# Kernel optimization log

Measured on AMD Instinct MI355X. Metric: run time of the kernel, lower is better.

## Reference

```python
import jax, jax.numpy as jnp
import numpy as np

B, N = 1, 512
CS, CZ = 384, 128
H, DQK, DV, PQK, PV = 12, 16, 16, 4, 8
EPS = 1e-8
SW = float(np.sqrt(1.0 / (3 * DQK)))            # scalar_weights
PW = float(np.sqrt(1.0 / (3 * PQK * 9.0 / 2)))  # point_weights
ZW = float(np.sqrt(1.0 / 3))                    # attention_2d_weights


def _lin(key, din, dout):
    return 0.02 * jax.random.normal(key, (din, dout), dtype=jnp.float32), jnp.zeros((dout,), dtype=jnp.float32)


def setup_inputs():
    key = jax.random.key(0)
    ks = jax.random.split(key, 16)
    Wsq, bsq = _lin(ks[0], CS, H * DQK)
    Wsk, bsk = _lin(ks[1], CS, H * DQK)
    Wsv, bsv = _lin(ks[2], CS, H * DV)
    Wsb, bsb = _lin(ks[3], CZ, H)
    Wpq, bpq = _lin(ks[4], CS, H * PQK * 3)
    Wpk, bpk = _lin(ks[5], CS, H * PQK * 3)
    Wpv, bpv = _lin(ks[6], CS, H * PV * 3)
    Wout, bout = _lin(ks[7], H * (DV + PV * 4 + CZ), CS)
    w_attn = 0.5 * jax.random.normal(ks[8], (3,), dtype=jnp.float32)  # attn_linear weight (1,3)
    b_attn = jnp.zeros((), dtype=jnp.float32)
    tpw = jnp.full((H,), float(np.log(np.e - 1.0)), dtype=jnp.float32)  # trainable_point_weight
    s = jax.random.normal(ks[9], (B, N, CS), dtype=jnp.float32)
    z = jax.random.normal(ks[10], (B, N, N, CZ), dtype=jnp.float32)
    rot = jax.random.normal(ks[11], (B, N, 3, 3), dtype=jnp.float32)
    tran = jax.random.normal(ks[12], (B, N, 3), dtype=jnp.float32)
    res_mask = jnp.ones((B, N), dtype=jnp.float32)
    return dict(s=s, z=z, rot=rot, tran=tran, res_mask=res_mask,
                Wsq=Wsq, bsq=bsq, Wsk=Wsk, bsk=bsk, Wsv=Wsv, bsv=bsv,
                Wsb=Wsb, bsb=bsb, Wpq=Wpq, bpq=bpq, Wpk=Wpk, bpk=bpk,
                Wpv=Wpv, bpv=bpv, w_attn=w_attn, b_attn=b_attn, tpw=tpw,
                Wout=Wout, bout=bout)


def _ipa(s, z, rot, tran, res_mask, Wsq, bsq, Wsk, bsk, Wsv, bsv, Wsb, bsb,
         Wpq, bpq, Wpk, bpk, Wpv, bpv, w_attn, b_attn, tpw, Wout, bout):
    b, n, _ = s.shape
    sq = (s @ Wsq + bsq).reshape(b, n, H, DQK)
    sk = (s @ Wsk + bsk).reshape(b, n, H, DQK)
    sv = (s @ Wsv + bsv).reshape(b, n, H, DV)
    sb = z @ Wsb + bsb  # [b, i, j, h] pair bias

    def to_global(W, bias, p):
        t = (s @ W + bias).reshape(b, n, H, p, 3)
        return jnp.einsum('bnxy,bnhpy->bnhpx', rot, t) + tran[:, :, None, None, :]

    pqg = to_global(Wpq, bpq, PQK)
    pkg = to_global(Wpk, bpk, PQK)
    pvg = to_global(Wpv, bpv, PV)

    diff = pqg[:, :, None] - pkg[:, None, :]          # [b, i, j, h, p, 3]
    sdist = jnp.sum(diff * diff, axis=(-1, -2))       # [b, i, j, h]

    attn_point = -0.5 * jax.nn.softplus(tpw) * sdist * PW
    attn_scalar = jnp.einsum('bihd,bjhd->bijh', sq * SW, sk)
    attn_pair = sb * ZW
    # attn_linear(stack([scalar, point, pair], -1)).squeeze(-1)
    logits = attn_scalar * w_attn[0] + attn_point * w_attn[1] + attn_pair * w_attn[2] + b_attn

    mask2d = res_mask[:, :, None] * res_mask[:, None, :]
    logits = jnp.where(mask2d[..., None] == 0, jnp.finfo(logits.dtype).min, logits)
    attn = jax.nn.softmax(logits, axis=2)             # softmax over j

    r_scalar = jnp.einsum('bijh,bjhd->bihd', attn, sv)
    r_pt_g = jnp.einsum('bijh,bjhpc->bihpc', attn, pvg)
    # rotate back to local frame: R^T (x - t)
    r_pt = jnp.einsum('biyx,bihpy->bihpx', rot, r_pt_g - tran[:, :, None, None, :])
    r_norm = jnp.sqrt(jnp.sum(r_pt * r_pt, axis=-1) + EPS)  # [b, i, h, p]
    r_pair = jnp.einsum('bijh,bijc->bihc', attn, z)

    cat = jnp.concatenate([r_scalar, r_pt.reshape(b, n, H, PV * 3), r_norm, r_pair], axis=-1)
    return cat.reshape(b, n, -1) @ Wout + bout


def reference(s, z, rot, tran, res_mask, Wsq, bsq, Wsk, bsk, Wsv, bsv, Wsb, bsb,
              Wpq, bpq, Wpk, bpk, Wpv, bpv, w_attn, b_attn, tpw, Wout, bout):
    return _ipa(s, z, rot, tran, res_mask, Wsq, bsq, Wsk, bsk, Wsv, bsv, Wsb, bsb,
                Wpq, bpq, Wpk, bpk, Wpv, bpv, w_attn, b_attn, tpw, Wout, bout)
```

## Files before the change

kernel.cpp:

```cpp
#include <hip/hip_runtime.h>
#include <hip/hip_bf16.h>
#include <math.h>

#define NN 512
#define CSD 384
#define CZ 128
#define HH 12
#define TMPW 1152
#define CATH 176
#define CATDIM 2112
#define NSPLIT 6
#define KSPL 352

#define SW 0.14433756729740643f
#define PW 0.13608276348795434f
#define ZW 0.57735026918962576f
#define NEG_INF -3.4028234663852886e38f

typedef float f32x4_t __attribute__((ext_vector_type(4)));
typedef short bf16x8_t __attribute__((ext_vector_type(8)));

union BFU { uint4 q; bf16x8_t v; ushort u[8]; };

static __device__ __forceinline__ ushort f2bf(float f) {
    __hip_bfloat16 h = __float2bfloat16(f);
    return *reinterpret_cast<ushort*>(&h);
}
static __device__ __forceinline__ float bf2f(ushort u) {
    unsigned int v = ((unsigned int)u) << 16;
    return __uint_as_float(v);
}

__global__ void proj_gemm_kernel(const float* __restrict__ s, const float* __restrict__ rot,
                                 const float* __restrict__ tran,
                                 const float* __restrict__ Wsq, const float* __restrict__ bsq,
                                 const float* __restrict__ Wsk, const float* __restrict__ bsk,
                                 const float* __restrict__ Wsv, const float* __restrict__ bsv,
                                 const float* __restrict__ Wpq, const float* __restrict__ bpq,
                                 const float* __restrict__ Wpk, const float* __restrict__ bpk,
                                 const float* __restrict__ Wpv, const float* __restrict__ bpv,
                                 float* __restrict__ tmp)
{
    int bx = blockIdx.x;
    int n0 = blockIdx.y * 32;
    int f0 = bx * 48;
    const float* W; const float* bb; int dout; int segstart;
    if (bx < 4)       { W = Wsq; bb = bsq; dout = 192; segstart = 0; }
    else if (bx < 8)  { W = Wsk; bb = bsk; dout = 192; segstart = 192; }
    else if (bx < 12) { W = Wsv; bb = bsv; dout = 192; segstart = 384; }
    else if (bx < 15) { W = Wpq; bb = bpq; dout = 144; segstart = 576; }
    else if (bx < 18) { W = Wpk; bb = bpk; dout = 144; segstart = 720; }
    else              { W = Wpv; bb = bpv; dout = 288; segstart = 864; }
    int colbase = f0 - segstart;

    __shared__ float St[32][34];
    __shared__ float Ws[32][49];
    int tid = threadIdx.x;
    int ty = tid >> 4, tx = tid & 15;
    float acc[2][3] = {{0,0,0},{0,0,0}};

    for (int k0 = 0; k0 < CSD; k0 += 32) {
        {
            int r = tid >> 3, c4 = (tid & 7) * 4;
            float4 v = *(const float4*)&s[(size_t)(n0 + r) * CSD + k0 + c4];
            St[c4 + 0][r] = v.x; St[c4 + 1][r] = v.y; St[c4 + 2][r] = v.z; St[c4 + 3][r] = v.w;
        }
        for (int e = tid; e < 1536; e += 256) {
            int r = e / 48, c = e % 48;
            Ws[r][c] = W[(size_t)(k0 + r) * dout + colbase + c];
        }
        __syncthreads();
        #pragma unroll
        for (int k = 0; k < 32; k++) {
            float2 a = *(const float2*)&St[k][ty * 2];
            float b0 = Ws[k][tx * 3], b1 = Ws[k][tx * 3 + 1], b2 = Ws[k][tx * 3 + 2];
            acc[0][0] += a.x * b0; acc[0][1] += a.x * b1; acc[0][2] += a.x * b2;
            acc[1][0] += a.y * b0; acc[1][1] += a.y * b1; acc[1][2] += a.y * b2;
        }
        __syncthreads();
    }
    float bv0 = bb[colbase + tx * 3], bv1 = bb[colbase + tx * 3 + 1], bv2 = bb[colbase + tx * 3 + 2];
    #pragma unroll
    for (int r = 0; r < 2; r++) {
        int n = n0 + ty * 2 + r;
        float v0 = acc[r][0] + bv0, v1 = acc[r][1] + bv1, v2 = acc[r][2] + bv2;
        float* o = tmp + (size_t)n * TMPW + f0 + tx * 3;
        if (bx >= 12) {
            const float* R = rot + n * 9;
            const float* T = tran + n * 3;
            float g0 = R[0] * v0 + R[1] * v1 + R[2] * v2 + T[0];
            float g1 = R[3] * v0 + R[4] * v1 + R[5] * v2 + T[1];
            float g2 = R[6] * v0 + R[7] * v1 + R[8] * v2 + T[2];
            o[0] = g0; o[1] = g1; o[2] = g2;
        } else {
            o[0] = v0; o[1] = v1; o[2] = v2;
        }
    }
}

__global__ void augprep_kernel(const float* __restrict__ tmp,
                               const float* __restrict__ watt, const float* __restrict__ batt,
                               const float* __restrict__ tpw, const float* __restrict__ bsb,
                               ushort* __restrict__ Qaug, ushort* __restrict__ Kaug)
{
    int n = blockIdx.x;
    int tid = threadIdx.x;
    float w0 = watt[0], w1 = watt[1], w2 = watt[2], ba = batt[0];
    float A2 = w2 * ZW;
    __shared__ float nq[12], nk[12];
    if (tid < 24) {
        int h = tid >> 1, which = tid & 1;
        const float* p = tmp + (size_t)n * TMPW + (which ? 720 : 576) + h * 12;
        float s2 = 0.f;
        #pragma unroll
        for (int d = 0; d < 12; d++) s2 += p[d] * p[d];
        if (which) nk[h] = s2; else nq[h] = s2;
    }
    __syncthreads();

    for (int f = tid; f < 384; f += 256) {
        if (f < 192) {
            int h = f >> 4, k = f & 15;
            float sq = tmp[(size_t)n * TMPW + h * 16 + k] * (SW * w0);
            float sk = tmp[(size_t)n * TMPW + 192 + h * 16 + k];
            Qaug[((size_t)h * NN + n) * 32 + k] = f2bf(sq);
            Kaug[((size_t)h * NN + n) * 32 + k] = f2bf(sk);
        } else if (f < 336) {
            int e = f - 192; int h = e / 12, d = e % 12;
            float cpt = -0.5f * log1pf(expf(tpw[h])) * PW * w1;
            float pq = tmp[(size_t)n * TMPW + 576 + h * 12 + d];
            float pk = tmp[(size_t)n * TMPW + 720 + h * 12 + d];
            Qaug[((size_t)h * NN + n) * 32 + 16 + d] = f2bf(-2.f * cpt * pq);
            Kaug[((size_t)h * NN + n) * 32 + 16 + d] = f2bf(pk);
        } else {
            int e = f - 336; int h = e >> 2, sl = e & 3;
            float cpt = -0.5f * log1pf(expf(tpw[h])) * PW * w1;
            float qv, kv;
            if (sl == 0)      { qv = cpt * nq[h];      kv = 1.f; }
            else if (sl == 1) { qv = cpt;              kv = nk[h]; }
            else if (sl == 2) { qv = A2 * bsb[h] + ba; kv = 1.f; }
            else              { qv = 0.f;              kv = 0.f; }
            Qaug[((size_t)h * NN + n) * 32 + 28 + sl] = f2bf(qv);
            Kaug[((size_t)h * NN + n) * 32 + 28 + sl] = f2bf(kv);
        }
    }
}

__global__ __launch_bounds__(256) void zlogits_kernel(const float* __restrict__ z,
                                                      const float* __restrict__ resm,
                                                      const float* __restrict__ Wsb,
                                                      const float* __restrict__ watt,
                                                      float* __restrict__ lgts)
{
    int jc = blockIdx.x;
    int i  = blockIdx.y;
    int tid = threadIdx.x;
    int w = tid >> 6, lane = tid & 63;
    int l16 = lane & 15, lhi = lane >> 4;
    float A2 = watt[2] * ZW;

    BFU breg[4];
    #pragma unroll
    for (int kk = 0; kk < 4; kk++) {
        #pragma unroll
        for (int e = 0; e < 8; e++) {
            int k = kk * 32 + lhi * 8 + e;
            float v = (l16 < HH) ? Wsb[k * HH + l16] * A2 : 0.f;
            breg[kk].u[e] = f2bf(v);
        }
    }

    const float* zi = z + (size_t)i * NN * CZ;
    float rmi = resm[i];

    #pragma unroll
    for (int t = 0; t < 2; t++) {
        int jbase = jc * 128 + (w * 2 + t) * 16;
        const float* zr = zi + (size_t)(jbase + l16) * CZ + lhi * 8;
        float4 pr[8];
        #pragma unroll
        for (int kk = 0; kk < 4; kk++) {
            pr[kk * 2]     = *(const float4*)&zr[kk * 32];
            pr[kk * 2 + 1] = *(const float4*)&zr[kk * 32 + 4];
        }
        f32x4_t acc = {0.f, 0.f, 0.f, 0.f};
        #pragma unroll
        for (int kk = 0; kk < 4; kk++) {
            float4 f0 = pr[kk * 2], f1 = pr[kk * 2 + 1];
            BFU a;
            a.u[0] = f2bf(f0.x); a.u[1] = f2bf(f0.y); a.u[2] = f2bf(f0.z); a.u[3] = f2bf(f0.w);
            a.u[4] = f2bf(f1.x); a.u[5] = f2bf(f1.y); a.u[6] = f2bf(f1.z); a.u[7] = f2bf(f1.w);
            acc = __builtin_amdgcn_mfma_f32_16x16x32_bf16(a.v, breg[kk].v, acc, 0, 0, 0);
        }
        if (l16 < HH) {
            #pragma unroll
            for (int r = 0; r < 4; r++) {
                int j = jbase + lhi * 4 + r;
                float mj = rmi * resm[j];
                float lg = acc[r];
                if (mj == 0.f) lg = NEG_INF;
                lgts[((size_t)i * HH + l16) * NN + j] = lg;
            }
        }
    }
}

__global__ __launch_bounds__(256) void augsm_kernel(const float* __restrict__ lgts,
                                                    const ushort* __restrict__ Qaug,
                                                    const ushort* __restrict__ Kaug,
                                                    ushort* __restrict__ attn_bf)
{
    int it = blockIdx.x;
    int h  = blockIdx.y;
    __shared__ float Dt[16][520];
    int tid = threadIdx.x;
    int w = tid >> 6, lane = tid & 63;
    int l16 = lane & 15, lhi = lane >> 4;

    BFU a;
    a.q = *(const uint4*)&Qaug[(((size_t)h * NN) + it * 16 + l16) * 32 + lhi * 8];

    for (int jt = w; jt < 32; jt += 4) {
        BFU b;
        b.q = *(const uint4*)&Kaug[(((size_t)h * NN) + jt * 16 + l16) * 32 + lhi * 8];
        f32x4_t acc = {0.f, 0.f, 0.f, 0.f};
        acc = __builtin_amdgcn_mfma_f32_16x16x32_bf16(a.v, b.v, acc, 0, 0, 0);
        #pragma unroll
        for (int r = 0; r < 4; r++) Dt[lhi * 4 + r][jt * 16 + l16] = acc[r];
    }
    __syncthreads();

    #pragma unroll
    for (int rr = 0; rr < 4; rr++) {
        int row = w * 4 + rr;
        const float* lrow = lgts + (((size_t)(it * 16 + row)) * HH + h) * NN;
        float v[8]; float m = -INFINITY;
        #pragma unroll
        for (int u = 0; u < 8; u++) {
            v[u] = lrow[lane + 64 * u] + Dt[row][lane + 64 * u];
            m = fmaxf(m, v[u]);
        }
        for (int off = 32; off; off >>= 1) m = fmaxf(m, __shfl_xor(m, off));
        float ssum = 0.f;
        #pragma unroll
        for (int u = 0; u < 8; u++) { v[u] = __expf(v[u] - m); ssum += v[u]; }
        for (int off = 32; off; off >>= 1) ssum += __shfl_xor(ssum, off);
        float inv = 1.f / ssum;
        ushort* ag = attn_bf + (((size_t)(it * 16 + row)) * HH + h) * NN;
        #pragma unroll
        for (int u = 0; u < 8; u++) ag[lane + 64 * u] = f2bf(v[u] * inv);
    }
}

__global__ __launch_bounds__(256) void rpair_kernel(const float* __restrict__ z,
                                                    const ushort* __restrict__ attn_bf,
                                                    float* __restrict__ part)
{
    int jq = blockIdx.x;
    int i  = blockIdx.y;
    __shared__ ushort pbf[128 * 12];
    __shared__ float pslab[4 * 12 * 128];
    int tid = threadIdx.x;

    if (tid < 192) {
        int h = tid >> 4, g = tid & 15;
        BFU v; v.q = *(const uint4*)&attn_bf[((size_t)i * HH + h) * NN + jq * 128 + g * 8];
        #pragma unroll
        for (int q = 0; q < 8; q++) pbf[(g * 8 + q) * 12 + h] = v.u[q];
    }
    __syncthreads();

    int w = tid >> 6, lane = tid & 63;
    int c0 = lane * 2;
    const float* zq = z + ((size_t)i * NN + jq * 128 + w * 32) * CZ + c0;
    float acc[12][2];
    #pragma unroll
    for (int h = 0; h < 12; h++) { acc[h][0] = 0.f; acc[h][1] = 0.f; }

    #pragma unroll
    for (int j0 = 0; j0 < 32; j0 += 16) {
        float2 zv[16];
        #pragma unroll
        for (int u = 0; u < 16; u++) zv[u] = *(const float2*)&zq[(size_t)(j0 + u) * CZ];
        #pragma unroll
        for (int u = 0; u < 16; u++) {
            int jl = w * 32 + j0 + u;
            const uint2* pr = (const uint2*)&pbf[jl * 12];
            uint2 pa = pr[0], pb2 = pr[1], pc = pr[2];
            float ph[12];
            ph[0]  = bf2f((ushort)(pa.x & 0xffff)); ph[1]  = bf2f((ushort)(pa.x >> 16));
            ph[2]  = bf2f((ushort)(pa.y & 0xffff)); ph[3]  = bf2f((ushort)(pa.y >> 16));
            ph[4]  = bf2f((ushort)(pb2.x & 0xffff)); ph[5]  = bf2f((ushort)(pb2.x >> 16));
            ph[6]  = bf2f((ushort)(pb2.y & 0xffff)); ph[7]  = bf2f((ushort)(pb2.y >> 16));
            ph[8]  = bf2f((ushort)(pc.x & 0xffff)); ph[9]  = bf2f((ushort)(pc.x >> 16));
            ph[10] = bf2f((ushort)(pc.y & 0xffff)); ph[11] = bf2f((ushort)(pc.y >> 16));
            #pragma unroll
            for (int h = 0; h < 12; h++) {
                acc[h][0] += ph[h] * zv[u].x;
                acc[h][1] += ph[h] * zv[u].y;
            }
        }
    }
    #pragma unroll
    for (int h = 0; h < 12; h++)
        *(float2*)&pslab[(w * 12 + h) * 128 + c0] = make_float2(acc[h][0], acc[h][1]);
    __syncthreads();

    for (int e = tid; e < 1536; e += 256) {
        float ssum = pslab[e] + pslab[1536 + e] + pslab[3072 + e] + pslab[4608 + e];
        part[((size_t)jq * NN + i) * 1536 + e] = ssum;
    }
}

__global__ void combine_rpair_kernel(const float* __restrict__ part, float* __restrict__ cat)
{
    int v = blockIdx.x * 256 + threadIdx.x;
    int i = v / 1536, hc = v % 1536;
    int h = hc >> 7, c = hc & 127;
    float ssum = part[(size_t)i * 1536 + hc]
               + part[((size_t)NN + i) * 1536 + hc]
               + part[((size_t)2 * NN + i) * 1536 + hc]
               + part[((size_t)3 * NN + i) * 1536 + hc];
    cat[(size_t)i * CATDIM + h * CATH + 48 + c] = ssum;
}

__global__ void head_sum_kernel(const ushort* __restrict__ attn_bf, const float* __restrict__ tmp,
                                const float* __restrict__ rot, const float* __restrict__ tran,
                                float* __restrict__ cat)
{
    int i0 = blockIdx.x * 32;
    int h  = blockIdx.y;
    __shared__ float At[32][65];
    __shared__ float Sr[64][44];
    __shared__ float Rp[32][24];
    int tid = threadIdx.x;
    int il = tid & 31, fg = tid >> 5;
    float acc[5] = {0,0,0,0,0};

    for (int jc = 0; jc < NN; jc += 64) {
        {
            int r = tid >> 3, c8 = (tid & 7) * 8;
            const ushort* src = attn_bf + ((size_t)(i0 + r) * HH + h) * NN + jc + c8;
            BFU v; v.q = *(const uint4*)src;
            #pragma unroll
            for (int q = 0; q < 8; q++) At[r][c8 + q] = bf2f(v.u[q]);
        }
        {
            int jr = tid >> 2, d4 = (tid & 3) * 4;
            *(float4*)&Sr[jr][d4] = *(const float4*)&tmp[(size_t)(jc + jr) * TMPW + 384 + h * 16 + d4];
        }
        for (int e = tid; e < 384; e += 256) {
            int jr = e / 6, p4 = (e % 6) * 4;
            *(float4*)&Sr[jr][16 + p4] = *(const float4*)&tmp[(size_t)(jc + jr) * TMPW + 864 + h * 24 + p4];
        }
        __syncthreads();
        #pragma unroll 4
        for (int j = 0; j < 64; j++) {
            float a = At[il][j];
            #pragma unroll
            for (int q = 0; q < 5; q++) acc[q] += a * Sr[j][fg * 5 + q];
        }
        __syncthreads();
    }

    float* cbase = cat + (size_t)(i0 + il) * CATDIM + h * CATH;
    #pragma unroll
    for (int q = 0; q < 5; q++) {
        int f = fg * 5 + q;
        if (f < 16) cbase[f] = acc[q];
        else Rp[il][f - 16] = acc[q];
    }
    __syncthreads();

    {
        int il2 = tid >> 3, p = tid & 7;
        int i = i0 + il2;
        float gx = Rp[il2][p * 3 + 0] - tran[i * 3 + 0];
        float gy = Rp[il2][p * 3 + 1] - tran[i * 3 + 1];
        float gz = Rp[il2][p * 3 + 2] - tran[i * 3 + 2];
        const float* R = rot + i * 9;
        float lx = R[0] * gx + R[3] * gy + R[6] * gz;
        float ly = R[1] * gx + R[4] * gy + R[7] * gz;
        float lz = R[2] * gx + R[5] * gy + R[8] * gz;
        float nrm = sqrtf(lx * lx + ly * ly + lz * lz + 1e-8f);
        float* cp = cat + (size_t)i * CATDIM + h * CATH;
        cp[16 + p * 3 + 0] = lx; cp[16 + p * 3 + 1] = ly; cp[16 + p * 3 + 2] = lz;
        cp[40 + p] = nrm;
    }
}

__global__ void out_gemm_split_kernel(const float* __restrict__ cat, const float* __restrict__ Wout,
                                      float* __restrict__ part)
{
    int n0 = blockIdx.x * 64;
    int i0 = blockIdx.y * 64;
    int ks = blockIdx.z * KSPL;
    __shared__ float St[32][68];
    __shared__ float Bs[32][68];
    int tid = threadIdx.x;
    int ty = tid >> 4, tx = tid & 15;
    float acc[4][4] = {{0,0,0,0},{0,0,0,0},{0,0,0,0},{0,0,0,0}};

    for (int k0 = 0; k0 < KSPL; k0 += 32) {
        {
            int r = tid >> 2, c8 = (tid & 3) * 8;
            const float* src = cat + (size_t)(i0 + r) * CATDIM + ks + k0 + c8;
            float4 v0 = *(const float4*)src;
            float4 v1 = *(const float4*)(src + 4);
            St[c8+0][r]=v0.x; St[c8+1][r]=v0.y; St[c8+2][r]=v0.z; St[c8+3][r]=v0.w;
            St[c8+4][r]=v1.x; St[c8+5][r]=v1.y; St[c8+6][r]=v1.z; St[c8+7][r]=v1.w;
        }
        {
            int r = tid >> 3, c8 = (tid & 7) * 8;
            const float* src = Wout + (size_t)(ks + k0 + r) * CSD + n0 + c8;
            *(float4*)&Bs[r][c8]     = *(const float4*)src;
            *(float4*)&Bs[r][c8 + 4] = *(const float4*)(src + 4);
        }
        __syncthreads();
        #pragma unroll
        for (int k = 0; k < 32; k++) {
            float4 a = *(const float4*)&St[k][ty * 4];
            float4 b = *(const float4*)&Bs[k][tx * 4];
            float av[4] = {a.x, a.y, a.z, a.w};
            float bv[4] = {b.x, b.y, b.z, b.w};
            #pragma unroll
            for (int r = 0; r < 4; r++)
                #pragma unroll
                for (int c = 0; c < 4; c++) acc[r][c] += av[r] * bv[c];
        }
        __syncthreads();
    }
    #pragma unroll
    for (int r = 0; r < 4; r++) {
        float4 v = make_float4(acc[r][0], acc[r][1], acc[r][2], acc[r][3]);
        *(float4*)&part[((size_t)blockIdx.z * NN + i0 + ty * 4 + r) * CSD + n0 + tx * 4] = v;
    }
}

__global__ void reduce_out_kernel(const float* __restrict__ part, const float* __restrict__ bout,
                                  float* __restrict__ out)
{
    int v = blockIdx.x * 256 + threadIdx.x;
    int n4 = v % 96;
    float4 o = ((const float4*)bout)[n4];
    const float4* p4 = (const float4*)part;
    #pragma unroll
    for (int s = 0; s < NSPLIT; s++) {
        float4 t = p4[(size_t)s * 49152 + v];
        o.x += t.x; o.y += t.y; o.z += t.z; o.w += t.w;
    }
    ((float4*)out)[v] = o;
}

extern "C" void kernel_launch(void* const* d_in, const int* in_sizes, int n_in,
                              void* d_out, int out_size, void* d_ws, size_t ws_size,
                              hipStream_t stream) {
    const float* s    = (const float*)d_in[0];
    const float* z    = (const float*)d_in[1];
    const float* rot  = (const float*)d_in[2];
    const float* tran = (const float*)d_in[3];
    const float* resm = (const float*)d_in[4];
    const float* Wsq  = (const float*)d_in[5];  const float* bsq = (const float*)d_in[6];
    const float* Wsk  = (const float*)d_in[7];  const float* bsk = (const float*)d_in[8];
    const float* Wsv  = (const float*)d_in[9];  const float* bsv = (const float*)d_in[10];
    const float* Wsb  = (const float*)d_in[11]; const float* bsb = (const float*)d_in[12];
    const float* Wpq  = (const float*)d_in[13]; const float* bpq = (const float*)d_in[14];
    const float* Wpk  = (const float*)d_in[15]; const float* bpk = (const float*)d_in[16];
    const float* Wpv  = (const float*)d_in[17]; const float* bpv = (const float*)d_in[18];
    const float* watt = (const float*)d_in[19]; const float* batt = (const float*)d_in[20];
    const float* tpw  = (const float*)d_in[21];
    const float* Wout = (const float*)d_in[22]; const float* bout = (const float*)d_in[23];
    float* out = (float*)d_out;
    float* ws  = (float*)d_ws;

    float*  tmp     = ws;
    ushort* attn_bf = (ushort*)(ws + 589824);
    float*  lgts    = ws + 2162688;
    float*  partR   = ws + 5308416;
    ushort* Qaug    = (ushort*)(ws + 8454144);
    ushort* Kaug    = (ushort*)(ws + 8552448);
    float*  cat     = ws + 8650752;
    float*  partO   = ws + 9732096;

    proj_gemm_kernel<<<dim3(24, 16), 256, 0, stream>>>(s, rot, tran,
                                                       Wsq, bsq, Wsk, bsk, Wsv, bsv,
                                                       Wpq, bpq, Wpk, bpk, Wpv, bpv, tmp);
    augprep_kernel<<<512, 256, 0, stream>>>(tmp, watt, batt, tpw, bsb, Qaug, Kaug);
    zlogits_kernel<<<dim3(4, 512), 256, 0, stream>>>(z, resm, Wsb, watt, lgts);
    augsm_kernel<<<dim3(32, 12), 256, 0, stream>>>(lgts, Qaug, Kaug, attn_bf);
    rpair_kernel<<<dim3(4, 512), 256, 0, stream>>>(z, attn_bf, partR);
    combine_rpair_kernel<<<3072, 256, 0, stream>>>(partR, cat);
    head_sum_kernel<<<dim3(16, 12), 256, 0, stream>>>(attn_bf, tmp, rot, tran, cat);
    out_gemm_split_kernel<<<dim3(6, 8, NSPLIT), 256, 0, stream>>>(cat, Wout, partO);
    reduce_out_kernel<<<192, 256, 0, stream>>>(partO, bout, out);
}
```

Measured before the change: 184.3 us.

## Fuse pair-bias logits, softmax, and z-weighted pair reduction into flash-style kernel

The pair-bias logit computation, softmax, and attention-weighted reduction over z are merged into one online-softmax kernel. Each block reads its z rows once, keeps a running max and rescales its accumulators, then writes unnormalized exponentials, maxima and partial sums. A small combine kernel merges the two j-halves and normalizes. This removes the second full pass over the large z tensor and the float logits round-trip. In exchange there are more block syncs per tile, a serial scalar FMA loop over z, and bf16 storage of the scalar/point logits.

```diff
diff --git a/kernel.cpp b/kernel.cpp
--- a/kernel.cpp
+++ b/kernel.cpp
@@ -15,7 +15,7 @@
 #define SW 0.14433756729740643f
 #define PW 0.13608276348795434f
 #define ZW 0.57735026918962576f
-#define NEG_INF -3.4028234663852886e38f
+#define MASK_NEG -1.0e30f
 
 typedef float f32x4_t __attribute__((ext_vector_type(4)));
 typedef short bf16x8_t __attribute__((ext_vector_type(8)));
@@ -146,14 +146,56 @@
     }
 }
 
-__global__ __launch_bounds__(256) void zlogits_kernel(const float* __restrict__ z,
-                                                      const float* __restrict__ resm,
-                                                      const float* __restrict__ Wsb,
-                                                      const float* __restrict__ watt,
-                                                      float* __restrict__ lgts)
-{
-    int jc = blockIdx.x;
+__global__ __launch_bounds__(256) void sp_kernel(const ushort* __restrict__ Qaug,
+                                                 const ushort* __restrict__ Kaug,
+                                                 ushort* __restrict__ sp_bf)
+{
+    int it = blockIdx.x;
+    int h  = blockIdx.y;
+    __shared__ float Dt[16][520];
+    int tid = threadIdx.x;
+    int w = tid >> 6, lane = tid & 63;
+    int l16 = lane & 15, lhi = lane >> 4;
+
+    BFU a;
+    a.q = *(const uint4*)&Qaug[(((size_t)h * NN) + it * 16 + l16) * 32 + lhi * 8];
+
+    for (int jt = w; jt < 32; jt += 4) {
+        BFU b;
+        b.q = *(const uint4*)&Kaug[(((size_t)h * NN) + jt * 16 + l16) * 32 + lhi * 8];
+        f32x4_t acc = {0.f, 0.f, 0.f, 0.f};
+        acc = __builtin_amdgcn_mfma_f32_16x16x32_bf16(a.v, b.v, acc, 0, 0, 0);
+        #pragma unroll
+        for (int r = 0; r < 4; r++) Dt[lhi * 4 + r][jt * 16 + l16] = acc[r];
+    }
+    __syncthreads();
+
+    #pragma unroll
+    for (int rr = 0; rr < 4; rr++) {
+        int row = w * 4 + rr;
+        ushort* sp = sp_bf + (((size_t)(it * 16 + row)) * HH + h) * NN;
+        #pragma unroll
+        for (int u = 0; u < 8; u++) sp[lane + 64 * u] = f2bf(Dt[row][lane + 64 * u]);
+    }
+}
+
+__global__ __launch_bounds__(256) void flash_kernel(const float* __restrict__ z,
+                                                    const float* __restrict__ resm,
+                                                    const float* __restrict__ Wsb,
+                                                    const float* __restrict__ watt,
+                                                    const ushort* __restrict__ sp_bf,
+                                                    ushort* __restrict__ e_bf,
+                                                    float* __restrict__ partR,
+                                                    float* __restrict__ m_arr)
+{
+    int jh = blockIdx.x;
     int i  = blockIdx.y;
+    __shared__ float lt[256 * 13];
+    __shared__ float p_lds[64 * 13];
+    __shared__ ushort sp_lds[12 * 260];
+    __shared__ float mtile[4][12];
+    __shared__ float mrun[12];
+    __shared__ float scale_s[12];
     int tid = threadIdx.x;
     int w = tid >> 6, lane = tid & 63;
     int l16 = lane & 15, lhi = lane >> 4;
@@ -170,158 +212,134 @@
         }
     }
 
-    const float* zi = z + (size_t)i * NN * CZ;
+    for (int e = tid; e < 768; e += 256) {
+        int h = e >> 6, q = e & 63;
+        *(uint2*)&sp_lds[h * 260 + q * 4] =
+            *(const uint2*)&sp_bf[((size_t)i * HH + h) * NN + jh * 256 + q * 4];
+    }
+    if (tid < 12) mrun[tid] = -INFINITY;
+
+    int hg = tid >> 7, c = tid & 127;
+    float acc[6] = {0, 0, 0, 0, 0, 0};
     float rmi = resm[i];
-
-    #pragma unroll
-    for (int t = 0; t < 2; t++) {
-        int jbase = jc * 128 + (w * 2 + t) * 16;
-        const float* zr = zi + (size_t)(jbase + l16) * CZ + lhi * 8;
+    __syncthreads();
+
+    for (int t4 = 0; t4 < 4; t4++) {
+        int jloc = t4 * 64 + w * 16;
+        int jglob = jh * 256 + jloc;
+        const float* zr = z + ((size_t)i * NN + jglob + l16) * CZ + lhi * 8;
         float4 pr[8];
         #pragma unroll
         for (int kk = 0; kk < 4; kk++) {
             pr[kk * 2]     = *(const float4*)&zr[kk * 32];
             pr[kk * 2 + 1] = *(const float4*)&zr[kk * 32 + 4];
         }
-        f32x4_t acc = {0.f, 0.f, 0.f, 0.f};
+        f32x4_t a4 = {0.f, 0.f, 0.f, 0.f};
         #pragma unroll
         for (int kk = 0; kk < 4; kk++) {
             float4 f0 = pr[kk * 2], f1 = pr[kk * 2 + 1];
             BFU a;
             a.u[0] = f2bf(f0.x); a.u[1] = f2bf(f0.y); a.u[2] = f2bf(f0.z); a.u[3] = f2bf(f0.w);
             a.u[4] = f2bf(f1.x); a.u[5] = f2bf(f1.y); a.u[6] = f2bf(f1.z); a.u[7] = f2bf(f1.w);
-            acc = __builtin_amdgcn_mfma_f32_16x16x32_bf16(a.v, breg[kk].v, acc, 0, 0, 0);
+            a4 = __builtin_amdgcn_mfma_f32_16x16x32_bf16(a.v, breg[kk].v, a4, 0, 0, 0);
         }
         if (l16 < HH) {
+            float mw = -INFINITY;
             #pragma unroll
             for (int r = 0; r < 4; r++) {
-                int j = jbase + lhi * 4 + r;
-                float mj = rmi * resm[j];
-                float lg = acc[r];
-                if (mj == 0.f) lg = NEG_INF;
-                lgts[((size_t)i * HH + l16) * NN + j] = lg;
+                int jl = jloc + lhi * 4 + r;
+                float sp = bf2f(sp_lds[l16 * 260 + jl]);
+                float lg = a4[r] + sp;
+                if (rmi * resm[jh * 256 + jl] == 0.f) lg = MASK_NEG;
+                lt[jl * 13 + l16] = lg;
+                mw = fmaxf(mw, lg);
             }
-        }
-    }
-}
-
-__global__ __launch_bounds__(256) void augsm_kernel(const float* __restrict__ lgts,
-                                                    const ushort* __restrict__ Qaug,
-                                                    const ushort* __restrict__ Kaug,
-                                                    ushort* __restrict__ attn_bf)
-{
-    int it = blockIdx.x;
-    int h  = blockIdx.y;
-    __shared__ float Dt[16][520];
+            mw = fmaxf(mw, __shfl_xor(mw, 16));
+            mw = fmaxf(mw, __shfl_xor(mw, 32));
+            if (lhi == 0) mtile[w][l16] = mw;
+        }
+        __syncthreads();
+        if (tid < 12) {
+            float mo = mrun[tid];
+            float mn = fmaxf(mo, fmaxf(fmaxf(mtile[0][tid], mtile[1][tid]),
+                                       fmaxf(mtile[2][tid], mtile[3][tid])));
+            scale_s[tid] = (mo == -INFINITY) ? 0.f : __expf(mo - mn);
+            mrun[tid] = mn;
+        }
+        __syncthreads();
+        for (int e = tid; e < 768; e += 256) {
+            int jl = e & 63, h = e >> 6;
+            p_lds[jl * 13 + h] = __expf(lt[(t4 * 64 + jl) * 13 + h] - mrun[h]);
+        }
+        #pragma unroll
+        for (int q = 0; q < 6; q++) acc[q] *= scale_s[hg * 6 + q];
+        __syncthreads();
+        const float* z2 = z + ((size_t)i * NN + jh * 256 + t4 * 64) * CZ + c;
+        #pragma unroll 4
+        for (int jl = 0; jl < 64; jl++) {
+            float zv = z2[(size_t)jl * CZ];
+            #pragma unroll
+            for (int q = 0; q < 6; q++) acc[q] += p_lds[jl * 13 + hg * 6 + q] * zv;
+        }
+        __syncthreads();
+    }
+
+    for (int e = tid; e < 3072; e += 256) {
+        int jl = e & 255, h = e >> 8;
+        float ev = __expf(lt[jl * 13 + h] - mrun[h]);
+        e_bf[(((size_t)jh * NN + i) * HH + h) * 256 + jl] = f2bf(ev);
+    }
+    if (tid < 12) m_arr[((size_t)jh * NN + i) * HH + tid] = mrun[tid];
+    #pragma unroll
+    for (int q = 0; q < 6; q++)
+        partR[(((size_t)jh * NN + i) * HH + hg * 6 + q) * 128 + c] = acc[q];
+}
+
+__global__ __launch_bounds__(256) void combine_kernel(const ushort* __restrict__ e_bf,
+                                                      const float* __restrict__ m_arr,
+                                                      const float* __restrict__ partR,
+                                                      ushort* __restrict__ attn_bf,
+                                                      float* __restrict__ cat)
+{
+    int i = blockIdx.x;
+    __shared__ float sA[12], sB[12], invl[12];
     int tid = threadIdx.x;
     int w = tid >> 6, lane = tid & 63;
-    int l16 = lane & 15, lhi = lane >> 4;
-
-    BFU a;
-    a.q = *(const uint4*)&Qaug[(((size_t)h * NN) + it * 16 + l16) * 32 + lhi * 8];
-
-    for (int jt = w; jt < 32; jt += 4) {
-        BFU b;
-        b.q = *(const uint4*)&Kaug[(((size_t)h * NN) + jt * 16 + l16) * 32 + lhi * 8];
-        f32x4_t acc = {0.f, 0.f, 0.f, 0.f};
-        acc = __builtin_amdgcn_mfma_f32_16x16x32_bf16(a.v, b.v, acc, 0, 0, 0);
-        #pragma unroll
-        for (int r = 0; r < 4; r++) Dt[lhi * 4 + r][jt * 16 + l16] = acc[r];
+
+    #pragma unroll
+    for (int t = 0; t < 3; t++) {
+        int h = w * 3 + t;
+        float m0 = m_arr[((size_t)i) * HH + h];
+        float m1 = m_arr[((size_t)NN + i) * HH + h];
+        float m = fmaxf(m0, m1);
+        float s0 = __expf(m0 - m), s1 = __expf(m1 - m);
+        const ushort* e0 = e_bf + (((size_t)i) * HH + h) * 256;
+        const ushort* e1 = e_bf + (((size_t)NN + i) * HH + h) * 256;
+        float v0[4], v1[4]; float sum = 0.f;
+        #pragma unroll
+        for (int u = 0; u < 4; u++) {
+            v0[u] = bf2f(e0[lane + 64 * u]);
+            v1[u] = bf2f(e1[lane + 64 * u]);
+            sum += v0[u] * s0 + v1[u] * s1;
+        }
+        for (int off = 32; off; off >>= 1) sum += __shfl_xor(sum, off);
+        float inv = 1.f / sum;
+        ushort* ag = attn_bf + ((size_t)i * HH + h) * NN;
+        #pragma unroll
+        for (int u = 0; u < 4; u++) {
+            ag[lane + 64 * u]       = f2bf(v0[u] * s0 * inv);
+            ag[256 + lane + 64 * u] = f2bf(v1[u] * s1 * inv);
+        }
+        if (lane == 0) { sA[h] = s0; sB[h] = s1; invl[h] = inv; }
     }
     __syncthreads();
 
-    #pragma unroll
-    for (int rr = 0; rr < 4; rr++) {
-        int row = w * 4 + rr;
-        const float* lrow = lgts + (((size_t)(it * 16 + row)) * HH + h) * NN;
-        float v[8]; float m = -INFINITY;
-        #pragma unroll
-        for (int u = 0; u < 8; u++) {
-            v[u] = lrow[lane + 64 * u] + Dt[row][lane + 64 * u];
-            m = fmaxf(m, v[u]);
-        }
-        for (int off = 32; off; off >>= 1) m = fmaxf(m, __shfl_xor(m, off));
-        float ssum = 0.f;
-        #pragma unroll
-        for (int u = 0; u < 8; u++) { v[u] = __expf(v[u] - m); ssum += v[u]; }
-        for (int off = 32; off; off >>= 1) ssum += __shfl_xor(ssum, off);
-        float inv = 1.f / ssum;
-        ushort* ag = attn_bf + (((size_t)(it * 16 + row)) * HH + h) * NN;
-        #pragma unroll
-        for (int u = 0; u < 8; u++) ag[lane + 64 * u] = f2bf(v[u] * inv);
-    }
-}
-
-__global__ __launch_bounds__(256) void rpair_kernel(const float* __restrict__ z,
-                                                    const ushort* __restrict__ attn_bf,
-                                                    float* __restrict__ part)
-{
-    int jq = blockIdx.x;
-    int i  = blockIdx.y;
-    __shared__ ushort pbf[128 * 12];
-    __shared__ float pslab[4 * 12 * 128];
-    int tid = threadIdx.x;
-
-    if (tid < 192) {
-        int h = tid >> 4, g = tid & 15;
-        BFU v; v.q = *(const uint4*)&attn_bf[((size_t)i * HH + h) * NN + jq * 128 + g * 8];
-        #pragma unroll
-        for (int q = 0; q < 8; q++) pbf[(g * 8 + q) * 12 + h] = v.u[q];
-    }
-    __syncthreads();
-
-    int w = tid >> 6, lane = tid & 63;
-    int c0 = lane * 2;
-    const float* zq = z + ((size_t)i * NN + jq * 128 + w * 32) * CZ + c0;
-    float acc[12][2];
-    #pragma unroll
-    for (int h = 0; h < 12; h++) { acc[h][0] = 0.f; acc[h][1] = 0.f; }
-
-    #pragma unroll
-    for (int j0 = 0; j0 < 32; j0 += 16) {
-        float2 zv[16];
-        #pragma unroll
-        for (int u = 0; u < 16; u++) zv[u] = *(const float2*)&zq[(size_t)(j0 + u) * CZ];
-        #pragma unroll
-        for (int u = 0; u < 16; u++) {
-            int jl = w * 32 + j0 + u;
-            const uint2* pr = (const uint2*)&pbf[jl * 12];
-            uint2 pa = pr[0], pb2 = pr[1], pc = pr[2];
-            float ph[12];
-            ph[0]  = bf2f((ushort)(pa.x & 0xffff)); ph[1]  = bf2f((ushort)(pa.x >> 16));
-            ph[2]  = bf2f((ushort)(pa.y & 0xffff)); ph[3]  = bf2f((ushort)(pa.y >> 16));
-            ph[4]  = bf2f((ushort)(pb2.x & 0xffff)); ph[5]  = bf2f((ushort)(pb2.x >> 16));
-            ph[6]  = bf2f((ushort)(pb2.y & 0xffff)); ph[7]  = bf2f((ushort)(pb2.y >> 16));
-            ph[8]  = bf2f((ushort)(pc.x & 0xffff)); ph[9]  = bf2f((ushort)(pc.x >> 16));
-            ph[10] = bf2f((ushort)(pc.y & 0xffff)); ph[11] = bf2f((ushort)(pc.y >> 16));
-            #pragma unroll
-            for (int h = 0; h < 12; h++) {
-                acc[h][0] += ph[h] * zv[u].x;
-                acc[h][1] += ph[h] * zv[u].y;
-            }
-        }
-    }
-    #pragma unroll
-    for (int h = 0; h < 12; h++)
-        *(float2*)&pslab[(w * 12 + h) * 128 + c0] = make_float2(acc[h][0], acc[h][1]);
-    __syncthreads();
-
     for (int e = tid; e < 1536; e += 256) {
-        float ssum = pslab[e] + pslab[1536 + e] + pslab[3072 + e] + pslab[4608 + e];
-        part[((size_t)jq * NN + i) * 1536 + e] = ssum;
-    }
-}
-
-__global__ void combine_rpair_kernel(const float* __restrict__ part, float* __restrict__ cat)
-{
-    int v = blockIdx.x * 256 + threadIdx.x;
-    int i = v / 1536, hc = v % 1536;
-    int h = hc >> 7, c = hc & 127;
-    float ssum = part[(size_t)i * 1536 + hc]
-               + part[((size_t)NN + i) * 1536 + hc]
-               + part[((size_t)2 * NN + i) * 1536 + hc]
-               + part[((size_t)3 * NN + i) * 1536 + hc];
-    cat[(size_t)i * CATDIM + h * CATH + 48 + c] = ssum;
+        int h = e >> 7, c = e & 127;
+        float v = (partR[(((size_t)i) * HH + h) * 128 + c] * sA[h]
+                 + partR[(((size_t)NN + i) * HH + h) * 128 + c] * sB[h]) * invl[h];
+        cat[(size_t)i * CATDIM + h * CATH + 48 + c] = v;
+    }
 }
 
 __global__ void head_sum_kernel(const ushort* __restrict__ attn_bf, const float* __restrict__ tmp,
@@ -475,21 +493,23 @@
 
     float*  tmp     = ws;
     ushort* attn_bf = (ushort*)(ws + 589824);
-    float*  lgts    = ws + 2162688;
+    ushort* sp_bf   = (ushort*)(ws + 2162688);
+    ushort* e_bf    = (ushort*)(ws + 3735552);
     float*  partR   = ws + 5308416;
-    ushort* Qaug    = (ushort*)(ws + 8454144);
-    ushort* Kaug    = (ushort*)(ws + 8552448);
-    float*  cat     = ws + 8650752;
-    float*  partO   = ws + 9732096;
+    float*  m_arr   = ws + 6881280;
+    ushort* Qaug    = (ushort*)(ws + 6893568);
+    ushort* Kaug    = (ushort*)(ws + 6991872);
+    float*  cat     = ws + 7090176;
+    float*  partO   = ws + 8171520;
 
     proj_gemm_kernel<<<dim3(24, 16), 256, 0, stream>>>(s, rot, tran,
                                                        Wsq, bsq, Wsk, bsk, Wsv, bsv,
                                                        Wpq, bpq, Wpk, bpk, Wpv, bpv, tmp);
     augprep_kernel<<<512, 256, 0, stream>>>(tmp, watt, batt, tpw, bsb, Qaug, Kaug);
-    zlogits_kernel<<<dim3(4, 512), 256, 0, stream>>>(z, resm, Wsb, watt, lgts);
-    augsm_kernel<<<dim3(32, 12), 256, 0, stream>>>(lgts, Qaug, Kaug, attn_bf);
-    rpair_kernel<<<dim3(4, 512), 256, 0, stream>>>(z, attn_bf, partR);
-    combine_rpair_kernel<<<3072, 256, 0, stream>>>(partR, cat);
+    sp_kernel<<<dim3(32, 12), 256, 0, stream>>>(Qaug, Kaug, sp_bf);
+    flash_kernel<<<dim3(2, 512), 256, 0, stream>>>(z, resm, Wsb, watt, sp_bf,
+                                                   e_bf, partR, m_arr);
+    combine_kernel<<<512, 256, 0, stream>>>(e_bf, m_arr, partR, attn_bf, cat);
     head_sum_kernel<<<dim3(16, 12), 256, 0, stream>>>(attn_bf, tmp, rot, tran, cat);
     out_gemm_split_kernel<<<dim3(6, 8, NSPLIT), 256, 0, stream>>>(cat, Wout, partO);
     reduce_out_kernel<<<192, 256, 0, stream>>>(partO, bout, out);
```

Result: faster. 160.5 us (-12.9%).
